# Optimization experiments

Hardware: AMD Instinct MI355X
Metric: run time of the kernel (lower is better)

## Reference

```python
import math
import jax, jax.numpy as jnp
import numpy as np

B, S, D, H = 2, 2048, 1024, 16


def setup_inputs() -> dict:
    key = jax.random.key(0)
    ks = jax.random.split(key, 8)
    scale = 1.0 / math.sqrt(D)
    kv_mask = jax.random.randint(ks[1], (B, S), 0, 2).astype(bool)
    kv_mask = kv_mask.at[:, 0].set(True)  # ensure at least one valid kv per batch
    return {
        "q": jax.random.normal(ks[0], (B, S, D), dtype=jnp.float32),
        "kv_mask": kv_mask,
        "Wq": jax.random.normal(ks[2], (D, D), dtype=jnp.float32) * scale,
        "Wk": jax.random.normal(ks[3], (D, D), dtype=jnp.float32) * scale,
        "Wv": jax.random.normal(ks[4], (D, D), dtype=jnp.float32) * scale,
        "Wo": jax.random.normal(ks[5], (D, D), dtype=jnp.float32) * scale,
        "bo": jax.random.normal(ks[6], (D,), dtype=jnp.float32) * 0.01,
        "num_heads": H,
    }


def _pass_with_mask(x, W, mask, b=None):
    # Linear applied everywhere, output zeroed where mask is False (pass_with_mask)
    y = x @ W.T
    if b is not None:
        y = y + b
    return jnp.where(mask[..., None], y, 0.0)


def reference(q, kv_mask, Wq, Wk, Wv, Wo, bo, num_heads):
    b, s, d = q.shape
    hd = d // num_heads
    q_mask = jnp.ones((b, s), dtype=bool)  # default q_mask in the module
    # self-attention: k = v = q
    qh = _pass_with_mask(q, Wq, q_mask).reshape(b, s, num_heads, hd)
    kh = _pass_with_mask(q, Wk, kv_mask).reshape(b, s, num_heads, hd)
    vh = _pass_with_mask(q, Wv, kv_mask).reshape(b, s, num_heads, hd)
    # scores: note the module scales by sqrt(model_dim), NOT sqrt(head_dim)
    scores = jnp.einsum("bqhd,bkhd->bhqk", qh, kh) / math.sqrt(d)
    mask = (q_mask[:, :, None] & kv_mask[:, None, :])[:, None, :, :]  # [b,1,q,k]
    scores = jnp.where(mask, scores, -jnp.inf)
    attn = jax.nn.softmax(scores, axis=-1)
    attn = jnp.where(mask, attn, 0.0)
    out = jnp.einsum("bhqk,bkhd->bqhd", attn, vh).reshape(b, s, d)
    return _pass_with_mask(out, Wo, q_mask, bo)
```

## Files before the change

### kernel.cpp

```cpp
#include <hip/hip_runtime.h>
#include <math.h>

#define B_ 2
#define S_ 2048
#define DM 1024
#define NH 16
#define HD 64

typedef unsigned short u16;
typedef unsigned int u32;
typedef __attribute__((ext_vector_type(8))) short bf16x8;
typedef __attribute__((ext_vector_type(4))) float f32x4;

#define C2SCALE 0.0450842200277800f

__device__ __forceinline__ u16 f2bf(float x) {
  unsigned u = __float_as_uint(x);
  u = (u + 0x7FFFu + ((u >> 16) & 1u)) >> 16;
  return (u16)u;
}

__device__ __forceinline__ u32 cvtpk(float lo, float hi) {
  u32 r;
  asm("v_cvt_pk_bf16_f32 %0, %1, %2" : "=v"(r) : "v"(lo), "v"(hi));
  return r;
}

__device__ __forceinline__ float exp2a(float x) {
  float r;
  asm("v_exp_f32 %0, %1" : "=v"(r) : "v"(x));
  return r;
}

__device__ __forceinline__ void gload_lds16(const u16* g, u16* l) {
  __builtin_amdgcn_global_load_lds((const __attribute__((address_space(1))) void*)g,
                                   (__attribute__((address_space(3))) void*)l, 16, 0, 0);
}

__device__ __forceinline__ int sigpos(int w6) {
  return ((w6 >> 5) << 5) | (((w6 >> 2) & 3) << 3) | (((w6 >> 4) & 1) << 2) | (w6 & 3);
}

__global__ void mask_scan(const int* __restrict__ kvm, int* __restrict__ posb,
                          int* __restrict__ nvb, u16* __restrict__ mwg) {
  const int b = blockIdx.x;
  const int tid = threadIdx.x;
  const int lane = tid & 63, wv = tid >> 6;
  __shared__ int wsum[4];
  int v[8], s = 0;
  const int base = b * S_ + tid * 8;
#pragma unroll
  for (int j = 0; j < 8; j++) { v[j] = kvm[base + j] ? 1 : 0; s += v[j]; }
  int sc = s;
#pragma unroll
  for (int off = 1; off < 64; off <<= 1) {
    int t = __shfl_up(sc, off, 64);
    if (lane >= off) sc += t;
  }
  if (lane == 63) wsum[wv] = sc;
  __syncthreads();
  int woff = 0;
#pragma unroll
  for (int w = 0; w < 4; w++) woff += (w < wv) ? wsum[w] : 0;
  int run = woff + sc - s;
#pragma unroll
  for (int j = 0; j < 8; j++) { posb[base + j] = run; run += v[j]; }
  const int total = wsum[0] + wsum[1] + wsum[2] + wsum[3];
  if (tid == 0) nvb[b] = total;
  for (int i = tid; i < S_; i += 256)
    mwg[b * S_ + (i & ~63) + sigpos(i & 63)] = (i < total) ? 0xFFFFu : 0u;
}

__global__ void cvt_all(const float* __restrict__ q, const float* __restrict__ Wq,
                        const float* __restrict__ Wk, const float* __restrict__ Wv,
                        const float* __restrict__ Wo, const int* __restrict__ nvb,
                        u16* __restrict__ Xbf, u16* __restrict__ Wcat,
                        u16* __restrict__ Wobf, u16* __restrict__ vtbuf) {
  const int NQ4 = (B_ * S_ * DM) / 4;
  const int NW4 = (DM * DM) / 4;
  const int total = NQ4 + 4 * NW4;
  int i = blockIdx.x * blockDim.x + threadIdx.x;
  int stride = gridDim.x * blockDim.x;
  for (int idx = i; idx < B_ * NH * HD * 64; idx += stride) {
    int col = idx & 63;
    int dd = (idx >> 6) & 63;
    int bh = idx >> 12;
    int nv = nvb[bh >> 4];
    int padw = ((nv + 63) & ~63) - nv;
    if (col < padw)
      vtbuf[((size_t)bh * HD + dd) * S_ + nv + col] = 0;
  }
  for (; i < total; i += stride) {
    const float* src;
    u16* dst;
    if (i < NQ4) {
      src = q + (size_t)i * 4; dst = Xbf + (size_t)i * 4;
    } else {
      int t = i - NQ4;
      if (t < NW4)            { src = Wq + (size_t)t * 4; dst = Wcat + (size_t)t * 4; }
      else if (t < 2 * NW4)   { src = Wk + (size_t)(t - NW4) * 4;     dst = Wcat + DM * DM + (size_t)(t - NW4) * 4; }
      else if (t < 3 * NW4)   { src = Wv + (size_t)(t - 2 * NW4) * 4; dst = Wcat + 2 * DM * DM + (size_t)(t - 2 * NW4) * 4; }
      else                    { src = Wo + (size_t)(t - 3 * NW4) * 4; dst = Wobf + (size_t)(t - 3 * NW4) * 4; }
    }
    float4 v = *(const float4*)src;
    ushort4 o;
    o.x = f2bf(v.x); o.y = f2bf(v.y); o.z = f2bf(v.z); o.w = f2bf(v.w);
    *(ushort4*)dst = o;
  }
}

__global__ __launch_bounds__(256, 2) void gemm_bt(
    const u16* __restrict__ A, const u16* __restrict__ Bw, int K,
    u16* __restrict__ qo, u16* __restrict__ ko, u16* __restrict__ vo,
    const int* __restrict__ kvm, const int* __restrict__ posb) {
  __shared__ __align__(16) u16 As[128 * 32];
  __shared__ __align__(16) u16 Bs[128 * 32];
  const int tid = threadIdx.x;
  const int wv = tid >> 6, lane = tid & 63;
  const int g = lane >> 4, c = lane & 15;
  const int wr = wv >> 1, wc = wv & 1;
  const int L = blockIdx.y * gridDim.x + blockIdx.x;
  const int cpx = (gridDim.x * gridDim.y) >> 3;
  const int Ls = (L & 7) * cpx + (L >> 3);
  const int Mb = (Ls & 31) << 7, Nb = (Ls >> 5) << 7;

  f32x4 acc[4][4];
#pragma unroll
  for (int i = 0; i < 4; i++)
#pragma unroll
    for (int j = 0; j < 4; j++) acc[i][j] = f32x4{0.f, 0.f, 0.f, 0.f};

  for (int kb = 0; kb < K; kb += 32) {
#pragma unroll
    for (int it = 0; it < 2; ++it) {
      int id = it * 256 + tid;
      int m = id >> 2, kk = (id & 3) * 8;
      gload_lds16(A + (size_t)(Mb + m) * K + kb + kk, As + (it * 4 + wv) * 512);
      gload_lds16(Bw + (size_t)(Nb + m) * K + kb + kk, Bs + (it * 4 + wv) * 512);
    }
    __syncthreads();
    bf16x8 af[4], bfr[4];
#pragma unroll
    for (int mi = 0; mi < 4; mi++)
      af[mi] = *(const bf16x8*)(As + (wr * 64 + mi * 16 + c) * 32 + g * 8);
#pragma unroll
    for (int ni = 0; ni < 4; ni++)
      bfr[ni] = *(const bf16x8*)(Bs + (wc * 64 + ni * 16 + c) * 32 + g * 8);
#pragma unroll
    for (int mi = 0; mi < 4; mi++)
#pragma unroll
      for (int ni = 0; ni < 4; ni++)
        acc[mi][ni] = __builtin_amdgcn_mfma_f32_16x16x32_bf16(af[mi], bfr[ni], acc[mi][ni], 0, 0, 0);
    __syncthreads();
  }

  const int nbase = Nb + wc * 64 + c;
  const int which = nbase >> 10;
  if (which == 0) {
#pragma unroll
    for (int mi = 0; mi < 4; mi++) {
#pragma unroll
      for (int ni = 0; ni < 4; ni++) {
        int nn = nbase + ni * 16;
        int h = nn >> 6, d = nn & 63;
#pragma unroll
        for (int r = 0; r < 4; r++) {
          int row = Mb + wr * 64 + mi * 16 + g * 4 + r;
          int b0 = row >> 11, s0 = row & 2047;
          qo[(((size_t)(b0 * NH + h)) * S_ + s0) * HD + d] =
              f2bf(acc[mi][ni][r] * C2SCALE);
        }
      }
    }
  } else if (which == 1) {
#pragma unroll
    for (int mi = 0; mi < 4; mi++) {
#pragma unroll
      for (int r = 0; r < 4; r++) {
        int row = Mb + wr * 64 + mi * 16 + g * 4 + r;
        int b0 = row >> 11, s0 = row & 2047;
        if (kvm[b0 * S_ + s0]) {
          int p = posb[b0 * S_ + s0];
#pragma unroll
          for (int ni = 0; ni < 4; ni++) {
            int nn = (nbase + ni * 16) & 1023;
            ko[((size_t)(b0 * NH + (nn >> 6)) * S_ + p) * HD + (nn & 63)] =
                f2bf(acc[mi][ni][r]);
          }
        }
      }
    }
  } else {
#pragma unroll
    for (int mi = 0; mi < 4; mi++) {
#pragma unroll
      for (int r = 0; r < 4; r++) {
        int row = Mb + wr * 64 + mi * 16 + g * 4 + r;
        int b0 = row >> 11, s0 = row & 2047;
        if (kvm[b0 * S_ + s0]) {
          int p = posb[b0 * S_ + s0];
          int dst = (p & ~63) + sigpos(p & 63);
#pragma unroll
          for (int ni = 0; ni < 4; ni++) {
            int nn = (nbase + ni * 16) & 1023;
            vo[((size_t)((b0 * NH + (nn >> 6)) * HD + (nn & 63))) * S_ + dst] =
                f2bf(acc[mi][ni][r]);
          }
        }
      }
    }
  }
}

__global__ __launch_bounds__(256, 4) void gemm_n64(
    const u16* __restrict__ A, const u16* __restrict__ Bw,
    const float* __restrict__ bias, float* __restrict__ fo) {
  __shared__ __align__(16) u16 As[128 * 32];
  __shared__ __align__(16) u16 Bs[64 * 32];
  const int K = DM, N = DM;
  const int tid = threadIdx.x;
  const int wv = tid >> 6, lane = tid & 63;
  const int g = lane >> 4, c = lane & 15;
  const int wr = wv >> 1, wc = wv & 1;
  const int L = blockIdx.x;
  const int Ls = (L & 7) * 64 + (L >> 3);
  const int Mb = (Ls & 31) << 7, Nb = (Ls >> 5) << 6;

  f32x4 acc[4][2];
#pragma unroll
  for (int i = 0; i < 4; i++)
#pragma unroll
    for (int j = 0; j < 2; j++) acc[i][j] = f32x4{0.f, 0.f, 0.f, 0.f};

  for (int kb = 0; kb < K; kb += 32) {
#pragma unroll
    for (int it = 0; it < 2; ++it) {
      int id = it * 256 + tid;
      int m = id >> 2, kk = (id & 3) * 8;
      gload_lds16(A + (size_t)(Mb + m) * K + kb + kk, As + (it * 4 + wv) * 512);
    }
    {
      int m = tid >> 2, kk = (tid & 3) * 8;
      gload_lds16(Bw + (size_t)(Nb + m) * K + kb + kk, Bs + wv * 512);
    }
    __syncthreads();
    bf16x8 af[4], bfr[2];
#pragma unroll
    for (int mi = 0; mi < 4; mi++)
      af[mi] = *(const bf16x8*)(As + (wr * 64 + mi * 16 + c) * 32 + g * 8);
#pragma unroll
    for (int ni = 0; ni < 2; ni++)
      bfr[ni] = *(const bf16x8*)(Bs + (wc * 32 + ni * 16 + c) * 32 + g * 8);
#pragma unroll
    for (int mi = 0; mi < 4; mi++)
#pragma unroll
      for (int ni = 0; ni < 2; ni++)
        acc[mi][ni] = __builtin_amdgcn_mfma_f32_16x16x32_bf16(af[mi], bfr[ni], acc[mi][ni], 0, 0, 0);
    __syncthreads();
  }

#pragma unroll
  for (int mi = 0; mi < 4; mi++) {
#pragma unroll
    for (int ni = 0; ni < 2; ni++) {
      int n = Nb + wc * 32 + ni * 16 + c;
      float bv = bias[n];
#pragma unroll
      for (int r = 0; r < 4; r++) {
        int row = Mb + wr * 64 + mi * 16 + g * 4 + r;
        fo[(size_t)row * N + n] = acc[mi][ni][r] + bv;
      }
    }
  }
}

__global__ __launch_bounds__(512, 4) void attn_kernel(
    const u16* __restrict__ qb, const u16* __restrict__ kb,
    const u16* __restrict__ vtb, const u16* __restrict__ mwg,
    const int* __restrict__ nvb, u16* __restrict__ ob) {
  __shared__ __align__(16) u16 Kl[2][64 * 64];
  __shared__ __align__(16) u16 Vl[2][64 * 64];
  __shared__ __align__(16) u16 MW[S_];

  const int tid = threadIdx.x;
  const int wv = tid >> 6, lane = tid & 63;
  const int g = lane >> 4, c = lane & 15;

  const int L = blockIdx.x;
  const int j = L >> 3;
  const int bh = ((L & 7) << 2) | (j >> 4);
  const int qi = j & 15;
  const int b = bh >> 4, h = bh & 15;
  const int q0 = qi * 128;
  const size_t bhbase = (size_t)bh * (S_ * HD);
  const int NT = (nvb[b] + 63) >> 6;

  ((uint2*)MW)[tid] = ((const uint2*)(mwg + b * S_))[tid];

  bf16x8 qf[2];
#pragma unroll
  for (int ks = 0; ks < 2; ks++)
    qf[ks] = *(const bf16x8*)(qb + bhbase + (size_t)(q0 + wv * 16 + c) * HD + ks * 32 + g * 8);

  f32x4 Oa[4];
#pragma unroll
  for (int di = 0; di < 4; di++) Oa[di] = f32x4{0.f, 0.f, 0.f, 0.f};
  f32x4 lacc = f32x4{0.f, 0.f, 0.f, 0.f};

  union { u32 u[4]; bf16x8 v; } ones;
#pragma unroll
  for (int w = 0; w < 4; w++) ones.u[w] = 0x3F803F80u;

  const int srow = tid >> 3;
  const int scol8 = tid & 7;
  const u16* kg = kb + bhbase + (size_t)srow * HD + scol8 * 8;
  const u16* vg = vtb + bhbase + (size_t)srow * S_ + scol8 * 8;
  const int wslot = scol8 ^ (srow & 7);
  u16* kld = &Kl[0][srow * 64 + wslot * 8];
  u16* vld = &Vl[0][srow * 64 + wslot * 8];

  bf16x8 krg = *(const bf16x8*)kg;
  bf16x8 vrg = *(const bf16x8*)vg;
  *(bf16x8*)kld = krg;
  *(bf16x8*)vld = vrg;
  krg = *(const bf16x8*)(kg + 64 * HD);
  vrg = *(const bf16x8*)(vg + 64);
  __syncthreads();

  const int swz = c & 7;

  for (int t = 0; t < NT; ++t) {
    const int cur = t & 1;
    if (t + 1 < NT) {
      *(bf16x8*)(kld + (cur ^ 1) * 4096) = krg;
      *(bf16x8*)(vld + (cur ^ 1) * 4096) = vrg;
      if (t + 2 < NT) {
        krg = *(const bf16x8*)(kg + (t + 2) * (64 * HD));
        vrg = *(const bf16x8*)(vg + (t + 2) * 64);
      }
    }
    const u16* KB = &Kl[cur][0];
    const u16* VB = &Vl[cur][0];

    f32x4 Sa[4];
#pragma unroll
    for (int ni = 0; ni < 4; ni++) Sa[ni] = f32x4{0.f, 0.f, 0.f, 0.f};
    __builtin_amdgcn_s_setprio(1);
#pragma unroll
    for (int ks = 0; ks < 2; ks++) {
      bf16x8 kf[4];
#pragma unroll
      for (int ni = 0; ni < 4; ni++)
        kf[ni] = *(const bf16x8*)&KB[(ni * 16 + c) * 64 + (((4 * ks + g) ^ swz) * 8)];
#pragma unroll
      for (int ni = 0; ni < 4; ni++)
        Sa[ni] = __builtin_amdgcn_mfma_f32_16x16x32_bf16(kf[ni], qf[ks], Sa[ni], 0, 0, 0);
    }
    __builtin_amdgcn_s_setprio(0);

    bf16x8 Pa[2];
#pragma unroll
    for (int ks = 0; ks < 2; ks++) {
      uint4 mw = *(const uint4*)&MW[t * 64 + ks * 32 + g * 8];
      union { u32 u[4]; bf16x8 v; } pw;
      pw.u[0] = cvtpk(exp2a(Sa[2 * ks][0]), exp2a(Sa[2 * ks][1])) & mw.x;
      pw.u[1] = cvtpk(exp2a(Sa[2 * ks][2]), exp2a(Sa[2 * ks][3])) & mw.y;
      pw.u[2] = cvtpk(exp2a(Sa[2 * ks + 1][0]), exp2a(Sa[2 * ks + 1][1])) & mw.z;
      pw.u[3] = cvtpk(exp2a(Sa[2 * ks + 1][2]), exp2a(Sa[2 * ks + 1][3])) & mw.w;
      Pa[ks] = pw.v;
    }

    __builtin_amdgcn_s_setprio(1);
    lacc = __builtin_amdgcn_mfma_f32_16x16x32_bf16(ones.v, Pa[0], lacc, 0, 0, 0);
    lacc = __builtin_amdgcn_mfma_f32_16x16x32_bf16(ones.v, Pa[1], lacc, 0, 0, 0);
#pragma unroll
    for (int ks = 0; ks < 2; ks++) {
      bf16x8 vf[4];
#pragma unroll
      for (int di = 0; di < 4; di++)
        vf[di] = *(const bf16x8*)&VB[(di * 16 + c) * 64 + (((4 * ks + g) ^ swz) * 8)];
#pragma unroll
      for (int di = 0; di < 4; di++)
        Oa[di] = __builtin_amdgcn_mfma_f32_16x16x32_bf16(vf[di], Pa[ks], Oa[di], 0, 0, 0);
    }
    __builtin_amdgcn_s_setprio(0);

    asm volatile("s_waitcnt lgkmcnt(0)\n\ts_barrier" ::: "memory");
  }

  float inv = 1.f / lacc[0];
  int q = q0 + wv * 16 + c;
  size_t base = ((size_t)(b * S_ + q)) * DM + (size_t)h * HD;
#pragma unroll
  for (int di = 0; di < 4; di++) {
    uint2 o;
    o.x = cvtpk(Oa[di][0] * inv, Oa[di][1] * inv);
    o.y = cvtpk(Oa[di][2] * inv, Oa[di][3] * inv);
    *(uint2*)(ob + base + di * 16 + g * 4) = o;
  }
}

extern "C" void kernel_launch(void* const* d_in, const int* in_sizes, int n_in,
                              void* d_out, int out_size, void* d_ws, size_t ws_size,
                              hipStream_t stream) {
  const float* q  = (const float*)d_in[0];
  const int* kvm  = (const int*)d_in[1];
  const float* Wq = (const float*)d_in[2];
  const float* Wk = (const float*)d_in[3];
  const float* Wv = (const float*)d_in[4];
  const float* Wo = (const float*)d_in[5];
  const float* bo = (const float*)d_in[6];
  float* out = (float*)d_out;
  char* ws = (char*)d_ws;

  u16* Xbf   = (u16*)(ws);
  u16* Wcat  = (u16*)(ws + (8u << 20));
  u16* Wobf  = (u16*)(ws + (14u << 20));
  u16* qbuf  = (u16*)(ws + (16u << 20));
  u16* kbuf  = (u16*)(ws + (24u << 20));
  u16* vtbuf = (u16*)(ws + (32u << 20));
  u16* mwg   = (u16*)(ws + (40u << 20));
  int* posb  = (int*)(ws + (41u << 20));
  int* nvb   = (int*)(ws + (42u << 20));
  u16* obuf  = Xbf;

  mask_scan<<<B_, 256, 0, stream>>>(kvm, posb, nvb, mwg);
  cvt_all<<<2048, 256, 0, stream>>>(q, Wq, Wk, Wv, Wo, nvb, Xbf, Wcat, Wobf, vtbuf);
  gemm_bt<<<dim3(32, 24), 256, 0, stream>>>(Xbf, Wcat, DM, qbuf, kbuf, vtbuf,
                                            kvm, posb);
  attn_kernel<<<512, 512, 0, stream>>>(qbuf, kbuf, vtbuf, mwg, nvb, obuf);
  gemm_n64<<<512, 256, 0, stream>>>(obuf, Wobf, bo, out);
}
```

Measured before the change: 109.1 us.

## Double-buffer QKV GEMM LDS tiles with register prefetch and swizzled layout

Replaces the direct global-to-LDS loads and two barriers per K step in the QKV projection GEMM with a register-staged, double-buffered LDS pipeline. Global loads for step t+2 are issued into registers while step t computes, and they are stored into the alternate LDS buffer, leaving one barrier per iteration. The LDS tile uses an XOR-swizzled 64-wide layout to avoid bank conflicts, and launch bounds are raised to 3 blocks per CU. The cost is extra registers and LDS per block, which may conflict with the higher occupancy target, plus a hand-written waitcnt/barrier.

```diff
diff --git a/kernel.cpp b/kernel.cpp
--- a/kernel.cpp
+++ b/kernel.cpp
@@ -109,12 +109,13 @@
   }
 }
 
-__global__ __launch_bounds__(256, 2) void gemm_bt(
-    const u16* __restrict__ A, const u16* __restrict__ Bw, int K,
+__global__ __launch_bounds__(256, 3) void gemm_bt(
+    const u16* __restrict__ A, const u16* __restrict__ Bw,
     u16* __restrict__ qo, u16* __restrict__ ko, u16* __restrict__ vo,
     const int* __restrict__ kvm, const int* __restrict__ posb) {
-  __shared__ __align__(16) u16 As[128 * 32];
-  __shared__ __align__(16) u16 Bs[128 * 32];
+  __shared__ __align__(16) u16 As[2][64 * 64];
+  __shared__ __align__(16) u16 Bs[2][64 * 64];
+  const int K = DM;
   const int tid = threadIdx.x;
   const int wv = tid >> 6, lane = tid & 63;
   const int g = lane >> 4, c = lane & 15;
@@ -130,28 +131,60 @@
 #pragma unroll
     for (int j = 0; j < 4; j++) acc[i][j] = f32x4{0.f, 0.f, 0.f, 0.f};
 
-  for (int kb = 0; kb < K; kb += 32) {
-#pragma unroll
-    for (int it = 0; it < 2; ++it) {
-      int id = it * 256 + tid;
-      int m = id >> 2, kk = (id & 3) * 8;
-      gload_lds16(A + (size_t)(Mb + m) * K + kb + kk, As + (it * 4 + wv) * 512);
-      gload_lds16(Bw + (size_t)(Nb + m) * K + kb + kk, Bs + (it * 4 + wv) * 512);
-    }
-    __syncthreads();
+  const int srow = tid >> 3;
+  const int scol8 = tid & 7;
+  const int m1 = srow * 2 + (scol8 >> 2);
+  const int kkc = (scol8 & 3) * 8;
+  const u16* ag1 = A + (size_t)(Mb + m1) * K + kkc;
+  const u16* ag2 = ag1 + (size_t)64 * K;
+  const u16* bg1 = Bw + (size_t)(Nb + m1) * K + kkc;
+  const u16* bg2 = bg1 + (size_t)64 * K;
+  const int slot = scol8 ^ (srow & 7);
+  u16* al1 = &As[0][srow * 64 + slot * 8];
+  u16* al2 = &As[0][(srow + 32) * 64 + slot * 8];
+  u16* bl1 = &Bs[0][srow * 64 + slot * 8];
+  u16* bl2 = &Bs[0][(srow + 32) * 64 + slot * 8];
+
+  bf16x8 ar0 = *(const bf16x8*)ag1, ar1 = *(const bf16x8*)ag2;
+  bf16x8 br0 = *(const bf16x8*)bg1, br1 = *(const bf16x8*)bg2;
+  *(bf16x8*)al1 = ar0; *(bf16x8*)al2 = ar1;
+  *(bf16x8*)bl1 = br0; *(bf16x8*)bl2 = br1;
+  ar0 = *(const bf16x8*)(ag1 + 32); ar1 = *(const bf16x8*)(ag2 + 32);
+  br0 = *(const bf16x8*)(bg1 + 32); br1 = *(const bf16x8*)(bg2 + 32);
+  __syncthreads();
+
+  const int off = ((((c & 1) << 2) | g) ^ (c >> 1)) << 3;
+  const int arb = (wr * 32 + (c >> 1)) * 64 + off;
+  const int brb = (wc * 32 + (c >> 1)) * 64 + off;
+
+  for (int t = 0; t < 32; ++t) {
+    const int cur = t & 1;
+    if (t + 1 < 32) {
+      const int nb = (cur ^ 1) * 4096;
+      *(bf16x8*)(al1 + nb) = ar0; *(bf16x8*)(al2 + nb) = ar1;
+      *(bf16x8*)(bl1 + nb) = br0; *(bf16x8*)(bl2 + nb) = br1;
+      if (t + 2 < 32) {
+        ar0 = *(const bf16x8*)(ag1 + (t + 2) * 32);
+        ar1 = *(const bf16x8*)(ag2 + (t + 2) * 32);
+        br0 = *(const bf16x8*)(bg1 + (t + 2) * 32);
+        br1 = *(const bf16x8*)(bg2 + (t + 2) * 32);
+      }
+    }
+    const u16* AB = &As[cur][0];
+    const u16* BB = &Bs[cur][0];
     bf16x8 af[4], bfr[4];
 #pragma unroll
     for (int mi = 0; mi < 4; mi++)
-      af[mi] = *(const bf16x8*)(As + (wr * 64 + mi * 16 + c) * 32 + g * 8);
+      af[mi] = *(const bf16x8*)&AB[arb + mi * 512];
 #pragma unroll
     for (int ni = 0; ni < 4; ni++)
-      bfr[ni] = *(const bf16x8*)(Bs + (wc * 64 + ni * 16 + c) * 32 + g * 8);
+      bfr[ni] = *(const bf16x8*)&BB[brb + ni * 512];
 #pragma unroll
     for (int mi = 0; mi < 4; mi++)
 #pragma unroll
       for (int ni = 0; ni < 4; ni++)
         acc[mi][ni] = __builtin_amdgcn_mfma_f32_16x16x32_bf16(af[mi], bfr[ni], acc[mi][ni], 0, 0, 0);
-    __syncthreads();
+    asm volatile("s_waitcnt lgkmcnt(0)\n\ts_barrier" ::: "memory");
   }
 
   const int nbase = Nb + wc * 64 + c;
@@ -426,7 +459,7 @@
 
   mask_scan<<<B_, 256, 0, stream>>>(kvm, posb, nvb, mwg);
   cvt_all<<<2048, 256, 0, stream>>>(q, Wq, Wk, Wv, Wo, nvb, Xbf, Wcat, Wobf, vtbuf);
-  gemm_bt<<<dim3(32, 24), 256, 0, stream>>>(Xbf, Wcat, DM, qbuf, kbuf, vtbuf,
+  gemm_bt<<<dim3(32, 24), 256, 0, stream>>>(Xbf, Wcat, qbuf, kbuf, vtbuf,
                                             kvm, posb);
   attn_kernel<<<512, 512, 0, stream>>>(qbuf, kbuf, vtbuf, mwg, nvb, obuf);
   gemm_n64<<<512, 256, 0, stream>>>(obuf, Wobf, bo, out);
```

Result: no change. 109.3 us (+0.2%).
